# Kernel optimization log

Hardware: AMD Instinct MI355X
Metric: run time of the kernel (lower is better)

Reference implementation:

```python
import jax, jax.numpy as jnp
import numpy as np

EPS = 1e-6
RES_CONN = True


def _layernorm(x, g, b):
    mu = jnp.mean(x, axis=-1, keepdims=True)
    var = jnp.var(x, axis=-1, keepdims=True)
    return (x - mu) * jax.lax.rsqrt(var + EPS) * g + b


def setup_inputs() -> dict:
    key = jax.random.key(0)
    ks = jax.random.split(key, 8)
    L, H, V, B, T = 2, 1024, 32000, 4, 512
    s = 0.02
    return {
        "x": jax.random.randint(ks[0], (B, T), 0, V, dtype=jnp.int32),
        "emb": jax.random.normal(ks[1], (V, H), jnp.float32) * s,
        "ln_g": jnp.ones((L, H), jnp.float32),
        "ln_b": jnp.zeros((L, H), jnp.float32),
        "Wl": jax.random.normal(ks[2], (L, 2 * H, 4 * H), jnp.float32) * s,
        "bl": jnp.zeros((L, 4 * H), jnp.float32),
        "Wo": jax.random.normal(ks[3], (L, H, H), jnp.float32) * s,
        "bo": jnp.zeros((L, H), jnp.float32),
        "W1": jax.random.normal(ks[4], (L, H, 4 * H), jnp.float32) * s,
        "b1": jnp.zeros((L, 4 * H), jnp.float32),
        "W2": jax.random.normal(ks[5], (L, 4 * H, H), jnp.float32) * s,
        "b2": jnp.zeros((L, H), jnp.float32),
    }


def reference(x, emb, ln_g, ln_b, Wl, bl, Wo, bo, W1, b1, W2, b2):
    # x: [B, T] int token ids. Returns dec_logits [B, T, V].
    B, T = x.shape
    L, H = ln_g.shape
    x_emb = emb[x]                      # [B, T, H] (dropout inactive: eval mode)
    xs = jnp.swapaxes(x_emb, 0, 1)      # [T, B, H]

    def step(carry, xt):
        c_prev, h_prev = carry          # each [L, B, H]
        cs, hs = [], []
        prev_input = jnp.zeros_like(xt)
        inp = xt                        # [B, H]
        for m in range(L):
            xn = _layernorm(inp, ln_g[m], ln_b[m])
            z = jnp.concatenate([xn, h_prev[m]], axis=-1) @ Wl[m] + bl[m]
            z = z.reshape(B, 4, H)
            i_g = jax.nn.sigmoid(z[:, 0])
            f_g = jax.nn.sigmoid(z[:, 1])
            o_g = jax.nn.sigmoid(z[:, 2])
            c = f_g * c_prev[m] + i_g * jnp.tanh(z[:, 3])
            h = o_g * jnp.tanh(c)
            ff = jax.nn.relu(xn @ W1[m] + b1[m]) @ W2[m] + b2[m]
            y = inp + ff + h @ Wo[m] + bo[m]
            if RES_CONN:
                y = y + prev_input
            prev_input = inp
            inp = y
            cs.append(c)
            hs.append(h)
        logits = inp @ emb.T            # tied embedding: [B, V]
        return (jnp.stack(cs), jnp.stack(hs)), logits

    carry0 = (jnp.zeros((L, B, H), x_emb.dtype), jnp.zeros((L, B, H), x_emb.dtype))
    _, logits = jax.lax.scan(step, carry0, xs)   # logits [T, B, V]
    return jnp.swapaxes(logits, 0, 1)            # [B, T, V]
```

## Files before the change

### kernel.cpp

```cpp
#include <hip/hip_runtime.h>

typedef unsigned short u16;
typedef short bf16x8 __attribute__((ext_vector_type(8)));
typedef unsigned short ushort8 __attribute__((ext_vector_type(8)));
typedef unsigned short us4 __attribute__((ext_vector_type(4)));
typedef unsigned u32x4 __attribute__((ext_vector_type(4)));
typedef float fx4 __attribute__((ext_vector_type(4)));

#define DEVI __device__ __forceinline__

enum { BB = 4, TT = 512, HH = 1024, VV = 32000, H4 = 4096 };
enum { WSTR = 1032 };

DEVI u16 f2bf(float f) {
    union { float f; unsigned u; } x; x.f = f;
    unsigned r = x.u + 0x7fff + ((x.u >> 16) & 1);
    return (u16)(r >> 16);
}
DEVI float bf2f(u16 u) {
    union { unsigned u; float f; } x; x.u = ((unsigned)u) << 16;
    return x.f;
}
DEVI float sigm(float x) { return 1.f / (1.f + __expf(-x)); }

DEVI unsigned ald_u32(const unsigned* p) { return __hip_atomic_load(p, __ATOMIC_RELAXED, __HIP_MEMORY_SCOPE_AGENT); }
DEVI void ast_u32(unsigned* p, unsigned v) { __hip_atomic_store(p, v, __ATOMIC_RELAXED, __HIP_MEMORY_SCOPE_AGENT); }

DEVI void ld4cc(const unsigned* p, u32x4* out) {
    asm volatile("global_load_dwordx4 %0, %1, off sc0 sc1" : "=v"(*out) : "v"(p));
}

DEVI void poll4096(const unsigned* base, unsigned want, u16* st, int tid) {
    const unsigned* p0 = base + tid * 8;
    const unsigned* p1 = p0 + 4;
    u32x4 v0, v1;
    ld4cc(p0, &v0); ld4cc(p1, &v1);
    asm volatile("s_waitcnt vmcnt(0)" ::: "memory");
    __builtin_amdgcn_sched_barrier(0);
    for (;;) {
        bool o0 = ((v0[0]>>16)==want)&((v0[1]>>16)==want)&((v0[2]>>16)==want)&((v0[3]>>16)==want);
        bool o1 = ((v1[0]>>16)==want)&((v1[1]>>16)==want)&((v1[2]>>16)==want)&((v1[3]>>16)==want);
        if (o0 & o1) break;
        __builtin_amdgcn_s_sleep(4);
        if (!o0) ld4cc(p0, &v0);
        if (!o1) ld4cc(p1, &v1);
        asm volatile("s_waitcnt vmcnt(0)" ::: "memory");
        __builtin_amdgcn_sched_barrier(0);
    }
    int wi = tid * 8;
    u16* d = st + (wi >> 10) * WSTR + (wi & 1023);
    *(us4*)d       = (us4){(u16)v0[0], (u16)v0[1], (u16)v0[2], (u16)v0[3]};
    *(us4*)(d + 4) = (us4){(u16)v1[0], (u16)v1[1], (u16)v1[2], (u16)v1[3]};
}

DEVI unsigned poll_word(const unsigned* p, unsigned want) {
    unsigned v = ald_u32(p);
    while ((v >> 16) != want) { __builtin_amdgcn_s_sleep(2); v = ald_u32(p); }
    return v & 0xFFFFu;
}

DEVI void gates64(const u16* wl, const u16* st, float* fb, int tid) {
    int lane = tid & 63, wv = tid >> 6;
    int rt = wv & 3, kh = wv >> 2;
    fx4 acc = {0.f, 0.f, 0.f, 0.f};
    int aoff = (rt * 16 + (lane & 15)) * WSTR + (lane >> 4) * 8;
    int boff = (lane & 3) * WSTR + (lane >> 4) * 8;
#pragma unroll
    for (int kt = 0; kt < 16; kt++) {
        int k0 = (kh * 16 + kt) * 32;
        bf16x8 a = *(const bf16x8*)(wl + aoff + k0);
        bf16x8 b = *(const bf16x8*)(st + boff + k0);
        acc = __builtin_amdgcn_mfma_f32_16x16x32_bf16(a, b, acc, 0, 0, 0);
    }
    int col = lane & 15;
    if (col < 4) {
        int r0 = rt * 16 + (lane >> 4) * 4;
#pragma unroll
        for (int ri = 0; ri < 4; ri++) fb[kh * 256 + (r0 + ri) * 4 + col] = acc[ri];
    }
}

__global__ void transpose_cast(const float* __restrict__ src, u16* __restrict__ dst, int R, int C) {
    __shared__ float tile[32][33];
    int c0 = blockIdx.x * 32, r0 = blockIdx.y * 32;
    int x = threadIdx.x, y = threadIdx.y;
#pragma unroll
    for (int i = 0; i < 32; i += 8) tile[y + i][x] = src[(size_t)(r0 + y + i) * C + c0 + x];
    __syncthreads();
#pragma unroll
    for (int i = 0; i < 32; i += 8) dst[(size_t)(c0 + y + i) * R + r0 + x] = f2bf(tile[x][y + i]);
}

__global__ void cast_bf16(const float* __restrict__ src, u16* __restrict__ dst, int n) {
    int i = blockIdx.x * 256 + threadIdx.x;
    if (i < n) dst[i] = f2bf(src[i]);
}

__global__ void zero_buf(float* p, int n) {
    int i = blockIdx.x * 256 + threadIdx.x;
    if (i < n) p[i] = 0.f;
}

__global__ __launch_bounds__(256) void gather_ln(const int* __restrict__ x, const float* __restrict__ emb,
                                                 const float* __restrict__ g, const float* __restrict__ b,
                                                 float* __restrict__ xe, u16* __restrict__ xn0) {
    int t = blockIdx.x, bb = blockIdx.y;
    int row = x[bb * TT + t];
    const float* e = emb + (size_t)row * HH;
    float v[4]; float s = 0.f, s2 = 0.f;
#pragma unroll
    for (int p = 0; p < 4; p++) { v[p] = e[p * 256 + threadIdx.x]; s += v[p]; s2 += v[p] * v[p]; }
    __shared__ float ls[4], ls2[4];
    for (int off = 32; off; off >>= 1) { s += __shfl_xor(s, off); s2 += __shfl_xor(s2, off); }
    int w = threadIdx.x >> 6, lane = threadIdx.x & 63;
    if (lane == 0) { ls[w] = s; ls2[w] = s2; }
    __syncthreads();
    s = ls[0] + ls[1] + ls[2] + ls[3];
    s2 = ls2[0] + ls2[1] + ls2[2] + ls2[3];
    float mu = s * (1.f / HH);
    float var = s2 * (1.f / HH) - mu * mu;
    float rs = rsqrtf(var + 1e-6f);
    size_t base = ((size_t)t * BB + bb) * HH;
#pragma unroll
    for (int p = 0; p < 4; p++) {
        int j = p * 256 + threadIdx.x;
        xe[base + j] = v[p];
        xn0[base + j] = f2bf((v[p] - mu) * rs * g[j] + b[j]);
    }
}

template <int MODE>
__global__ __launch_bounds__(256) void gemm_bt(const u16* __restrict__ A, const u16* __restrict__ Bt,
                                               float* __restrict__ Cf, u16* __restrict__ Cb,
                                               const float* __restrict__ bias, int M, int N, int K) {
    __shared__ u16 ldsA[128 * 40];
    __shared__ u16 ldsB[128 * 40];
    const int tid = threadIdx.x;
    const int m0 = blockIdx.y * 128, n0 = blockIdx.x * 128;
    const int lane = tid & 63, wid = tid >> 6;
    const int wr = wid >> 1, wc = wid & 1;
    const int l15 = lane & 15, lk = (lane >> 4) * 8;
    fx4 acc[4][4];
#pragma unroll
    for (int a = 0; a < 4; a++)
#pragma unroll
        for (int b = 0; b < 4; b++) { fx4 z = {0.f, 0.f, 0.f, 0.f}; acc[a][b] = z; }

    const int arow = tid >> 2, acol = (tid & 3) * 8;
    for (int k0 = 0; k0 < K; k0 += 32) {
#pragma unroll
        for (int p = 0; p < 2; p++) {
            int r = arow + p * 64;
            ushort8 va = *(const ushort8*)(A + (size_t)(m0 + r) * K + k0 + acol);
            *(ushort8*)&ldsA[r * 40 + acol] = va;
            ushort8 vb = *(const ushort8*)(Bt + (size_t)(n0 + r) * K + k0 + acol);
            *(ushort8*)&ldsB[r * 40 + acol] = vb;
        }
        __syncthreads();
        bf16x8 af[4], bfr[4];
#pragma unroll
        for (int mi = 0; mi < 4; mi++) af[mi] = *(const bf16x8*)&ldsA[(wr * 64 + mi * 16 + l15) * 40 + lk];
#pragma unroll
        for (int ni = 0; ni < 4; ni++) bfr[ni] = *(const bf16x8*)&ldsB[(wc * 64 + ni * 16 + l15) * 40 + lk];
#pragma unroll
        for (int mi = 0; mi < 4; mi++)
#pragma unroll
            for (int ni = 0; ni < 4; ni++)
                acc[mi][ni] = __builtin_amdgcn_mfma_f32_16x16x32_bf16(af[mi], bfr[ni], acc[mi][ni], 0, 0, 0);
        __syncthreads();
    }
#pragma unroll
    for (int mi = 0; mi < 4; mi++) {
#pragma unroll
        for (int ni = 0; ni < 4; ni++) {
#pragma unroll
            for (int r = 0; r < 4; r++) {
                int gr = m0 + wr * 64 + mi * 16 + (lane >> 4) * 4 + r;
                int gc = n0 + wc * 64 + ni * 16 + l15;
                float v = acc[mi][ni][r];
                if (MODE == 0) {
                    Cf[(size_t)gr * N + gc] = v + bias[gc];
                } else if (MODE == 1) {
                    float u = v + bias[gc];
                    Cb[(size_t)gr * N + gc] = f2bf(u > 0.f ? u : 0.f);
                } else if (MODE == 2) {
                    Cf[(size_t)gr * N + gc] += v;
                } else {
                    int b = gr & 3, t = gr >> 2;
                    Cf[((size_t)b * TT + t) * VV + gc] = v;
                }
            }
        }
    }
}

__global__ __launch_bounds__(512, 1) void lstm_pipe(
    const u16* __restrict__ Wh0T, const u16* __restrict__ Wo0T,
    const u16* __restrict__ Wx1T, const u16* __restrict__ Wh1T,
    const float* __restrict__ pz_all, const float* __restrict__ xe, const float* __restrict__ ff0,
    const float* __restrict__ lng, const float* __restrict__ lnb,
    const float* __restrict__ bl, const float* __restrict__ bo,
    float* __restrict__ y0_all, u16* __restrict__ xn1, u16* __restrict__ H1bf,
    unsigned* __restrict__ R) {
    __shared__ u16 wlds[64 * WSTR];
    __shared__ u16 stg[4 * WSTR];
    __shared__ float fb[1664];

    const int bid = blockIdx.x;
    const int tid = threadIdx.x;

    unsigned* RH0 = R;
    unsigned* RH1 = R + 32768;
    unsigned* RPART = R + 49152;
    unsigned* RXN = R + 53248;
    unsigned* RZX = R + 118784;
    unsigned* PROGY = R + 380928;
    unsigned* PROGZX = R + 382976;
    unsigned* PROGL1 = R + 385024;

    if (bid < 64) {
        const int w = bid;
        {
            int row = tid >> 3, kc = tid & 7;
            int gr = (row >> 4) * 1024 + w * 16 + (row & 15);
            const uint4* s = (const uint4*)(Wh0T + (size_t)gr * 1024 + kc * 128);
            uint4* d = (uint4*)(wlds + row * WSTR + kc * 128);
#pragma unroll
            for (int i = 0; i < 16; i++) d[i] = s[i];
        }
        if (tid < 64) fb[1024 + tid] = 0.f;
        __syncthreads();

        for (int s = 0; s < TT; s++) {
            if ((s & 3) == 0 && tid < 64) {
                for (;;) {
                    unsigned p = ald_u32(PROGY + tid * 32);
#pragma unroll
                    for (int off = 1; off < 64; off <<= 1) {
                        unsigned o = (unsigned)__shfl_xor((int)p, off);
                        p = p < o ? p : o;
                    }
                    if ((int)p >= s - 4) break;
                    __builtin_amdgcn_s_sleep(8);
                }
            }
            float pzv[4] = {0.f, 0.f, 0.f, 0.f};
            if (tid < 64) {
                int x = tid >> 2, b = tid & 3;
#pragma unroll
                for (int g = 0; g < 4; g++)
                    pzv[g] = pz_all[((size_t)s * 4 + b) * 4096 + g * 1024 + w * 16 + x];
            }
            poll4096(RH0 + ((s + 7) & 7) * 4096, (unsigned)s, stg, tid);
            __syncthreads();
            float* gbuf = fb + (s & 1) * 512;
            gates64(wlds, stg, gbuf, tid);
            __syncthreads();
            if (tid < 64) {
                int x = tid >> 2, b = tid & 3;
                float z0 = gbuf[(0*16+x)*4+b] + gbuf[256+(0*16+x)*4+b] + pzv[0];
                float z1 = gbuf[(1*16+x)*4+b] + gbuf[256+(1*16+x)*4+b] + pzv[1];
                float z2 = gbuf[(2*16+x)*4+b] + gbuf[256+(2*16+x)*4+b] + pzv[2];
                float z3 = gbuf[(3*16+x)*4+b] + gbuf[256+(3*16+x)*4+b] + pzv[3];
                float ig = sigm(z0), fg = sigm(z1), og = sigm(z2), gg = tanhf(z3);
                float c = fg * fb[1024 + tid] + ig * gg;
                fb[1024 + tid] = c;
                float h = og * tanhf(c);
                ast_u32(&RH0[(s & 7) * 4096 + b * 1024 + w * 16 + x],
                        ((unsigned)(s + 1) << 16) | f2bf(h));
            }
        }
    } else if (bid < 128) {
        const int wy = bid - 64;
        {
            int row = tid >> 5, kc = tid & 31;
            const uint4* s = (const uint4*)(Wo0T + (size_t)(wy * 16 + row) * 1024 + kc * 32);
            uint4* d = (uint4*)(wlds + row * WSTR + kc * 32);
            d[0] = s[0]; d[1] = s[1]; d[2] = s[2]; d[3] = s[3];
        }
        float lgR = 0.f, lbR = 0.f, boR = 0.f;
        if (tid < 64) {
            int x = tid >> 2;
            lgR = lng[1024 + wy * 16 + x];
            lbR = lnb[1024 + wy * 16 + x];
            boR = bo[wy * 16 + x];
        }
        __syncthreads();

        for (int t = 0; t <= TT; t++) {
            const bool doDot = (t < TT);
            const bool doLN = (t >= 1);
            if ((t & 7) == 0 && tid < 64) {
                for (;;) {
                    unsigned p = ald_u32(PROGZX + tid * 32);
#pragma unroll
                    for (int off = 1; off < 64; off <<= 1) {
                        unsigned o = (unsigned)__shfl_xor((int)p, off);
                        p = p < o ? p : o;
                    }
                    if ((int)p >= t - 8) break;
                    __builtin_amdgcn_s_sleep(8);
                }
            }
            float xev = 0.f, ffv = 0.f;
            if (doDot && tid < 64) {
                int x = tid >> 2, b = tid & 3;
                size_t base = ((size_t)t * 4 + b) * 1024 + wy * 16 + x;
                xev = xe[base]; ffv = ff0[base];
            }
            if (doDot) poll4096(RH0 + (t & 7) * 4096, (unsigned)(t + 1), stg, tid);
            __syncthreads();
            if (doDot && tid == 0) ast_u32(PROGY + wy * 32, (unsigned)(t + 1));
            if (doDot) {
                int out = tid >> 3, c = tid & 7;
                const u16* wrow = wlds + (out >> 2) * WSTR + c * 128;
                const u16* hrow = stg + (out & 3) * WSTR + c * 128;
                float acc = 0.f;
#pragma unroll
                for (int m = 0; m < 16; m++) {
                    ushort8 w8 = *(const ushort8*)(wrow + m * 8);
                    ushort8 h8 = *(const ushort8*)(hrow + m * 8);
#pragma unroll
                    for (int q = 0; q < 8; q++) acc += bf2f(w8[q]) * bf2f(h8[q]);
                }
                acc += __shfl_xor(acc, 1); acc += __shfl_xor(acc, 2); acc += __shfl_xor(acc, 4);
                if (c == 0) fb[512 + out] = acc;
            }
            if (doLN) {
                const unsigned* p = RPART + ((t - 1) & 3) * 1024 + tid * 2;
                unsigned hi = poll_word(p, (unsigned)t);
                unsigned lo = poll_word(p + 1, (unsigned)t);
                union { unsigned u; float f; } cv; cv.u = (hi << 16) | lo;
                fb[tid] = cv.f;
            }
            __syncthreads();
            if (doLN && tid < 8) {
                int b = tid & 3, kind = tid >> 2;
                float S = 0.f;
                for (int i = 0; i < 64; i++) S += fb[i * 8 + b * 2 + kind];
                fb[704 + kind * 4 + b] = S;
            }
            if (doDot && tid < 64) {
                int x = tid >> 2, b = tid & 3;
                float y = fb[512 + tid] + xev + ffv + boR;
                y0_all[((size_t)t * 4 + b) * 1024 + wy * 16 + x] = y;
                fb[576 + (t & 1) * 64 + tid] = y;
                float sv = y, sq = y * y;
#pragma unroll
                for (int off = 4; off < 64; off <<= 1) { sv += __shfl_xor(sv, off); sq += __shfl_xor(sq, off); }
                if (tid < 4) {
                    unsigned tg = (unsigned)(t + 1) << 16;
                    unsigned* pb = RPART + (t & 3) * 1024 + wy * 16 + tid * 4;
                    union { float f; unsigned u; } c1, c2; c1.f = sv; c2.f = sq;
                    ast_u32(pb + 0, tg | (c1.u >> 16));
                    ast_u32(pb + 1, tg | (c1.u & 0xFFFFu));
                    ast_u32(pb + 2, tg | (c2.u >> 16));
                    ast_u32(pb + 3, tg | (c2.u & 0xFFFFu));
                }
            }
            __syncthreads();
            if (doLN && tid < 64) {
                int x = tid >> 2, b = tid & 3;
                int u = t - 1;
                float mu = fb[704 + b] * (1.f / 1024.f);
                float rs = rsqrtf(fb[708 + b] * (1.f / 1024.f) - mu * mu + 1e-6f);
                float yv = fb[576 + (u & 1) * 64 + tid];
                float xnv = (yv - mu) * rs * lgR + lbR;
                u16 xb = f2bf(xnv);
                xn1[(size_t)u * 4096 + b * 1024 + wy * 16 + x] = xb;
                ast_u32(&RXN[(u & 15) * 4096 + b * 1024 + wy * 16 + x],
                        ((unsigned)(u + 1) << 16) | xb);
            }
        }
    } else if (bid < 192) {
        const int wz = bid - 128;
        {
            int row = tid >> 3, kc = tid & 7;
            int gr = (row >> 4) * 1024 + wz * 16 + (row & 15);
            const uint4* s = (const uint4*)(Wx1T + (size_t)gr * 1024 + kc * 128);
            uint4* d = (uint4*)(wlds + row * WSTR + kc * 128);
#pragma unroll
            for (int i = 0; i < 16; i++) d[i] = s[i];
        }
        if (tid < 64) fb[1536 + tid] = bl[4096 + (tid >> 4) * 1024 + wz * 16 + (tid & 15)];
        __syncthreads();

        for (int t = 0; t < TT; t++) {
            if ((t & 7) == 0 && tid == 0) {
                while ((int)ald_u32(PROGL1) < t - 6) __builtin_amdgcn_s_sleep(8);
            }
            poll4096(RXN + (t & 15) * 4096, (unsigned)(t + 1), stg, tid);
            __syncthreads();
            gates64(wlds, stg, fb, tid);
            __syncthreads();
            if (tid == 0) ast_u32(PROGZX + wz * 32, (unsigned)(t + 1));
            if (tid < 256) {
                int lr = tid >> 2, b = tid & 3;
                float v = fb[lr * 4 + b] + fb[256 + lr * 4 + b] + fb[1536 + lr];
                ast_u32(&RZX[(t & 15) * 16384 + wz * 256 + tid],
                        ((unsigned)(t + 1) << 16) | f2bf(v));
            }
            __syncthreads();
        }
    } else {
        const int w1 = bid - 192;
        {
            int row = tid >> 3, kc = tid & 7;
            int gr = (row >> 4) * 1024 + w1 * 16 + (row & 15);
            const uint4* s = (const uint4*)(Wh1T + (size_t)gr * 1024 + kc * 128);
            uint4* d = (uint4*)(wlds + row * WSTR + kc * 128);
#pragma unroll
            for (int i = 0; i < 16; i++) d[i] = s[i];
        }
        if (tid < 64) fb[1600 + tid] = 0.f;
        __syncthreads();

        for (int v = 0; v < TT; v++) {
            poll4096(RH1 + ((v + 3) & 3) * 4096, (unsigned)v, stg, tid);
            if (tid < 256) {
                const unsigned* p = RZX + (v & 15) * 16384 + w1 * 256 + tid;
                fb[1024 + (v & 1) * 256 + tid] = bf2f((u16)poll_word(p, (unsigned)(v + 1)));
            }
            __syncthreads();
            if (bid == 192 && tid == 0) ast_u32(PROGL1, (unsigned)(v + 1));
            float* gbuf = fb + (v & 1) * 512;
            gates64(wlds, stg, gbuf, tid);
            __syncthreads();
            if (tid < 64) {
                int x = tid >> 2, b = tid & 3;
                const float* zb = fb + 1024 + (v & 1) * 256;
                float z0 = gbuf[(0*16+x)*4+b] + gbuf[256+(0*16+x)*4+b] + zb[(0*16+x)*4+b];
                float z1 = gbuf[(1*16+x)*4+b] + gbuf[256+(1*16+x)*4+b] + zb[(1*16+x)*4+b];
                float z2 = gbuf[(2*16+x)*4+b] + gbuf[256+(2*16+x)*4+b] + zb[(2*16+x)*4+b];
                float z3 = gbuf[(3*16+x)*4+b] + gbuf[256+(3*16+x)*4+b] + zb[(3*16+x)*4+b];
                float ig = sigm(z0), fg = sigm(z1), og = sigm(z2), gg = tanhf(z3);
                float c = fg * fb[1600 + tid] + ig * gg;
                fb[1600 + tid] = c;
                float h = og * tanhf(c);
                u16 hb = f2bf(h);
                H1bf[(size_t)v * 4096 + b * 1024 + w1 * 16 + x] = hb;
                ast_u32(&RH1[(v & 3) * 4096 + b * 1024 + w1 * 16 + x],
                        ((unsigned)(v + 1) << 16) | hb);
            }
        }
    }
}

__global__ void p1_add(float* __restrict__ y, const float* __restrict__ xe,
                       const float* __restrict__ b2_1, const float* __restrict__ bo_1) {
    int idx = blockIdx.x * 256 + threadIdx.x;
    int j = idx & (HH - 1);
    y[idx] += xe[idx] + b2_1[j] + bo_1[j];
}

__global__ void p2_cast(const float* __restrict__ y, u16* __restrict__ o) {
    int idx = blockIdx.x * 256 + threadIdx.x;
    o[idx] = f2bf(y[idx]);
}

extern "C" void kernel_launch(void* const* d_in, const int* in_sizes, int n_in,
                              void* d_out, int out_size, void* d_ws, size_t ws_size,
                              hipStream_t stream) {
    const int* x = (const int*)d_in[0];
    const float* emb = (const float*)d_in[1];
    const float* ln_g = (const float*)d_in[2];
    const float* ln_b = (const float*)d_in[3];
    const float* Wl = (const float*)d_in[4];
    const float* bl = (const float*)d_in[5];
    const float* Wo = (const float*)d_in[6];
    const float* bo = (const float*)d_in[7];
    const float* W1 = (const float*)d_in[8];
    const float* b1 = (const float*)d_in[9];
    const float* W2 = (const float*)d_in[10];
    const float* b2 = (const float*)d_in[11];
    float* out = (float*)d_out;

    char* wp = (char*)d_ws;
    auto alloc = [&](size_t bytes) { void* p = wp; wp += (bytes + 255) & ~(size_t)255; return p; };
    const size_t MBT = (size_t)TT * BB;
    float* xe     = (float*)alloc(MBT * HH * 4);
    float* pre_z0 = (float*)alloc(MBT * H4 * 4);
    float* ff0    = (float*)alloc(MBT * HH * 4);
    float* y0_all = (float*)alloc(MBT * HH * 4);
    u16* xn0      = (u16*)alloc(MBT * HH * 2);
    u16* xn1      = (u16*)alloc(MBT * HH * 2);
    u16* U0       = (u16*)alloc(MBT * H4 * 2);
    u16* U1       = (u16*)alloc(MBT * H4 * 2);
    u16* H1bf     = (u16*)alloc(MBT * HH * 2);
    u16* Y1bf     = (u16*)alloc(MBT * HH * 2);
    unsigned* R   = (unsigned*)alloc(385056 * 4);
    u16* WlxT0 = (u16*)alloc((size_t)H4 * HH * 2);
    u16* WlhT0 = (u16*)alloc((size_t)H4 * HH * 2);
    u16* WlxT1 = (u16*)alloc((size_t)H4 * HH * 2);
    u16* WlhT1 = (u16*)alloc((size_t)H4 * HH * 2);
    u16* Wo0T  = (u16*)alloc((size_t)HH * HH * 2);
    u16* Wo1T  = (u16*)alloc((size_t)HH * HH * 2);
    u16* W10T  = (u16*)alloc((size_t)H4 * HH * 2);
    u16* W11T  = (u16*)alloc((size_t)H4 * HH * 2);
    u16* W20T  = (u16*)alloc((size_t)HH * H4 * 2);
    u16* W21T  = (u16*)alloc((size_t)HH * H4 * 2);
    u16* embB  = (u16*)alloc((size_t)VV * HH * 2);

    dim3 tb(32, 8);
    transpose_cast<<<dim3(128, 32), tb, 0, stream>>>(Wl, WlxT0, HH, H4);
    transpose_cast<<<dim3(128, 32), tb, 0, stream>>>(Wl + 1024 * 4096, WlhT0, HH, H4);
    transpose_cast<<<dim3(128, 32), tb, 0, stream>>>(Wl + 2048 * 4096, WlxT1, HH, H4);
    transpose_cast<<<dim3(128, 32), tb, 0, stream>>>(Wl + 3072 * 4096, WlhT1, HH, H4);
    transpose_cast<<<dim3(32, 32), tb, 0, stream>>>(Wo, Wo0T, HH, HH);
    transpose_cast<<<dim3(32, 32), tb, 0, stream>>>(Wo + 1024 * 1024, Wo1T, HH, HH);
    transpose_cast<<<dim3(128, 32), tb, 0, stream>>>(W1, W10T, HH, H4);
    transpose_cast<<<dim3(128, 32), tb, 0, stream>>>(W1 + 1024 * 4096, W11T, HH, H4);
    transpose_cast<<<dim3(32, 128), tb, 0, stream>>>(W2, W20T, H4, HH);
    transpose_cast<<<dim3(32, 128), tb, 0, stream>>>(W2 + 4096 * 1024, W21T, H4, HH);
    cast_bf16<<<(VV * HH + 255) / 256, 256, 0, stream>>>(emb, embB, VV * HH);
    gather_ln<<<dim3(TT, BB), 256, 0, stream>>>(x, emb, ln_g, ln_b, xe, xn0);

    gemm_bt<0><<<dim3(32, 16), 256, 0, stream>>>(xn0, WlxT0, pre_z0, nullptr, bl, 2048, 4096, 1024);
    gemm_bt<1><<<dim3(32, 16), 256, 0, stream>>>(xn0, W10T, nullptr, U0, b1, 2048, 4096, 1024);
    gemm_bt<0><<<dim3(8, 16), 256, 0, stream>>>(U0, W20T, ff0, nullptr, b2, 2048, 1024, 4096);

    zero_buf<<<1505, 256, 0, stream>>>((float*)R, 385056);

    lstm_pipe<<<256, 512, 0, stream>>>(WlhT0, Wo0T, WlxT1, WlhT1, pre_z0, xe, ff0,
                                       ln_g, ln_b, bl, bo, y0_all, xn1, H1bf, R);

    gemm_bt<1><<<dim3(32, 16), 256, 0, stream>>>(xn1, W11T, nullptr, U1, b1 + 4096, 2048, 4096, 1024);
    p1_add<<<8192, 256, 0, stream>>>(y0_all, xe, b2 + 1024, bo + 1024);
    gemm_bt<2><<<dim3(8, 16), 256, 0, stream>>>(U1, W21T, y0_all, nullptr, nullptr, 2048, 1024, 4096);
    gemm_bt<2><<<dim3(8, 16), 256, 0, stream>>>(H1bf, Wo1T, y0_all, nullptr, nullptr, 2048, 1024, 1024);
    p2_cast<<<8192, 256, 0, stream>>>(y0_all, Y1bf);
    gemm_bt<3><<<dim3(250, 16), 256, 0, stream>>>(Y1bf, embB, out, nullptr, nullptr, 2048, 32000, 1024);
}
```

Baseline: 3.693 ms.

## Replace per-element tagged h exchange with packed data plus per-block sentinel flags

Hidden-state exchange between LSTM blocks moves from per-element tagged 32-bit words (a step tag in the high half) to packed bf16 pairs plus a per-block sentinel array. Consumers poll 64 sentinels with one wave, then fetch the data once, instead of spin-polling all 4096 tagged words. This cuts polling traffic and halves the data size, at the cost of a store fence (waitcnt) before each sentinel write. It also deepens the ring buffer to 16 slots with a looser throttle, adds a custom tanh, tunes sleep intervals, and moves the Wo dot product after the layer-norm partial-sum wait so the two overlap.

```diff
diff --git a/kernel.cpp b/kernel.cpp
--- a/kernel.cpp
+++ b/kernel.cpp
@@ -22,6 +22,11 @@
     return x.f;
 }
 DEVI float sigm(float x) { return 1.f / (1.f + __expf(-x)); }
+DEVI float tanh_f(float x) {
+    float a = fabsf(x);
+    float t = 1.f - 2.f / (__expf(2.f * a) + 1.f);
+    return x < 0.f ? -t : t;
+}
 
 DEVI unsigned ald_u32(const unsigned* p) { return __hip_atomic_load(p, __ATOMIC_RELAXED, __HIP_MEMORY_SCOPE_AGENT); }
 DEVI void ast_u32(unsigned* p, unsigned v) { __hip_atomic_store(p, v, __ATOMIC_RELAXED, __HIP_MEMORY_SCOPE_AGENT); }
@@ -30,6 +35,24 @@
     asm volatile("global_load_dwordx4 %0, %1, off sc0 sc1" : "=v"(*out) : "v"(p));
 }
 
+template <int SLP>
+DEVI void sent_poll(const unsigned* sbase, unsigned want, int lane) {
+    const unsigned* p = sbase + lane;
+    unsigned v = ald_u32(p);
+    while (v != want) { __builtin_amdgcn_s_sleep(SLP); v = ald_u32(p); }
+}
+DEVI void data_fetch(const unsigned* dbase, u16* st, int tid) {
+    u32x4 d;
+    ld4cc(dbase + tid * 4, &d);
+    asm volatile("s_waitcnt vmcnt(0)" ::: "memory");
+    __builtin_amdgcn_sched_barrier(0);
+    int wi = tid * 8;
+    u16* dst = st + (wi >> 10) * WSTR + (wi & 1023);
+    *(us4*)dst       = (us4){(u16)d[0], (u16)(d[0] >> 16), (u16)d[1], (u16)(d[1] >> 16)};
+    *(us4*)(dst + 4) = (us4){(u16)d[2], (u16)(d[2] >> 16), (u16)d[3], (u16)(d[3] >> 16)};
+}
+
+template <int SLP>
 DEVI void poll4096(const unsigned* base, unsigned want, u16* st, int tid) {
     const unsigned* p0 = base + tid * 8;
     const unsigned* p1 = p0 + 4;
@@ -41,7 +64,7 @@
         bool o0 = ((v0[0]>>16)==want)&((v0[1]>>16)==want)&((v0[2]>>16)==want)&((v0[3]>>16)==want);
         bool o1 = ((v1[0]>>16)==want)&((v1[1]>>16)==want)&((v1[2]>>16)==want)&((v1[3]>>16)==want);
         if (o0 & o1) break;
-        __builtin_amdgcn_s_sleep(4);
+        __builtin_amdgcn_s_sleep(SLP);
         if (!o0) ld4cc(p0, &v0);
         if (!o1) ld4cc(p1, &v1);
         asm volatile("s_waitcnt vmcnt(0)" ::: "memory");
@@ -208,15 +231,18 @@
 
     const int bid = blockIdx.x;
     const int tid = threadIdx.x;
-
-    unsigned* RH0 = R;
-    unsigned* RH1 = R + 32768;
-    unsigned* RPART = R + 49152;
-    unsigned* RXN = R + 53248;
-    unsigned* RZX = R + 118784;
-    unsigned* PROGY = R + 380928;
-    unsigned* PROGZX = R + 382976;
-    unsigned* PROGL1 = R + 385024;
+    const int lane = tid & 63, wv = tid >> 6;
+
+    unsigned* RD0 = R;
+    unsigned* RS0 = R + 32768;
+    unsigned* RD1 = R + 33792;
+    unsigned* RS1 = R + 41984;
+    unsigned* RPART = R + 42240;
+    unsigned* RXN = R + 46336;
+    unsigned* RZX = R + 111872;
+    unsigned* PROGY = R + 374016;
+    unsigned* PROGZX = R + 376064;
+    unsigned* PROGL1 = R + 378112;
 
     if (bid < 64) {
         const int w = bid;
@@ -232,7 +258,7 @@
         __syncthreads();
 
         for (int s = 0; s < TT; s++) {
-            if ((s & 3) == 0 && tid < 64) {
+            if ((s & 7) == 0 && tid < 64) {
                 for (;;) {
                     unsigned p = ald_u32(PROGY + tid * 32);
 #pragma unroll
@@ -240,7 +266,7 @@
                         unsigned o = (unsigned)__shfl_xor((int)p, off);
                         p = p < o ? p : o;
                     }
-                    if ((int)p >= s - 4) break;
+                    if ((int)p >= s - 8) break;
                     __builtin_amdgcn_s_sleep(8);
                 }
             }
@@ -251,7 +277,9 @@
                 for (int g = 0; g < 4; g++)
                     pzv[g] = pz_all[((size_t)s * 4 + b) * 4096 + g * 1024 + w * 16 + x];
             }
-            poll4096(RH0 + ((s + 7) & 7) * 4096, (unsigned)s, stg, tid);
+            if (wv == 0) sent_poll<1>(RS0 + ((s + 15) & 15) * 64, (unsigned)s, lane);
+            __syncthreads();
+            data_fetch(RD0 + ((s + 15) & 15) * 2048, stg, tid);
             __syncthreads();
             float* gbuf = fb + (s & 1) * 512;
             gates64(wlds, stg, gbuf, tid);
@@ -262,12 +290,18 @@
                 float z1 = gbuf[(1*16+x)*4+b] + gbuf[256+(1*16+x)*4+b] + pzv[1];
                 float z2 = gbuf[(2*16+x)*4+b] + gbuf[256+(2*16+x)*4+b] + pzv[2];
                 float z3 = gbuf[(3*16+x)*4+b] + gbuf[256+(3*16+x)*4+b] + pzv[3];
-                float ig = sigm(z0), fg = sigm(z1), og = sigm(z2), gg = tanhf(z3);
+                float ig = sigm(z0), fg = sigm(z1), og = sigm(z2), gg = tanh_f(z3);
                 float c = fg * fb[1024 + tid] + ig * gg;
                 fb[1024 + tid] = c;
-                float h = og * tanhf(c);
-                ast_u32(&RH0[(s & 7) * 4096 + b * 1024 + w * 16 + x],
-                        ((unsigned)(s + 1) << 16) | f2bf(h));
+                float h = og * tanh_f(c);
+                float hn = __shfl(h, (tid + 4) & 63);
+                if (((tid >> 2) & 1) == 0) {
+                    int x = tid >> 2, b = tid & 3;
+                    unsigned word = (unsigned)f2bf(h) | ((unsigned)f2bf(hn) << 16);
+                    ast_u32(&RD0[(s & 15) * 2048 + b * 512 + w * 8 + (x >> 1)], word);
+                }
+                asm volatile("s_waitcnt vmcnt(0)" ::: "memory");
+                if (tid == 0) ast_u32(&RS0[(s & 15) * 64 + w], (unsigned)(s + 1));
             }
         }
     } else if (bid < 128) {
@@ -308,24 +342,9 @@
                 size_t base = ((size_t)t * 4 + b) * 1024 + wy * 16 + x;
                 xev = xe[base]; ffv = ff0[base];
             }
-            if (doDot) poll4096(RH0 + (t & 7) * 4096, (unsigned)(t + 1), stg, tid);
-            __syncthreads();
-            if (doDot && tid == 0) ast_u32(PROGY + wy * 32, (unsigned)(t + 1));
-            if (doDot) {
-                int out = tid >> 3, c = tid & 7;
-                const u16* wrow = wlds + (out >> 2) * WSTR + c * 128;
-                const u16* hrow = stg + (out & 3) * WSTR + c * 128;
-                float acc = 0.f;
-#pragma unroll
-                for (int m = 0; m < 16; m++) {
-                    ushort8 w8 = *(const ushort8*)(wrow + m * 8);
-                    ushort8 h8 = *(const ushort8*)(hrow + m * 8);
-#pragma unroll
-                    for (int q = 0; q < 8; q++) acc += bf2f(w8[q]) * bf2f(h8[q]);
-                }
-                acc += __shfl_xor(acc, 1); acc += __shfl_xor(acc, 2); acc += __shfl_xor(acc, 4);
-                if (c == 0) fb[512 + out] = acc;
-            }
+            if (doDot && wv == 0) sent_poll<4>(RS0 + (t & 15) * 64, (unsigned)(t + 1), lane);
+            __syncthreads();
+            if (doDot) data_fetch(RD0 + (t & 15) * 2048, stg, tid);
             if (doLN) {
                 const unsigned* p = RPART + ((t - 1) & 3) * 1024 + tid * 2;
                 unsigned hi = poll_word(p, (unsigned)t);
@@ -334,12 +353,29 @@
                 fb[tid] = cv.f;
             }
             __syncthreads();
+            if (doDot && tid == 0) ast_u32(PROGY + wy * 32, (unsigned)(t + 1));
             if (doLN && tid < 8) {
                 int b = tid & 3, kind = tid >> 2;
                 float S = 0.f;
                 for (int i = 0; i < 64; i++) S += fb[i * 8 + b * 2 + kind];
                 fb[704 + kind * 4 + b] = S;
             }
+            if (doDot) {
+                int out = tid >> 3, c = tid & 7;
+                const u16* wrow = wlds + (out >> 2) * WSTR + c * 128;
+                const u16* hrow = stg + (out & 3) * WSTR + c * 128;
+                float acc = 0.f;
+#pragma unroll
+                for (int m = 0; m < 16; m++) {
+                    ushort8 w8 = *(const ushort8*)(wrow + m * 8);
+                    ushort8 h8 = *(const ushort8*)(hrow + m * 8);
+#pragma unroll
+                    for (int q = 0; q < 8; q++) acc += bf2f(w8[q]) * bf2f(h8[q]);
+                }
+                acc += __shfl_xor(acc, 1); acc += __shfl_xor(acc, 2); acc += __shfl_xor(acc, 4);
+                if (c == 0) fb[512 + out] = acc;
+            }
+            __syncthreads();
             if (doDot && tid < 64) {
                 int x = tid >> 2, b = tid & 3;
                 float y = fb[512 + tid] + xev + ffv + boR;
@@ -389,7 +425,7 @@
             if ((t & 7) == 0 && tid == 0) {
                 while ((int)ald_u32(PROGL1) < t - 6) __builtin_amdgcn_s_sleep(8);
             }
-            poll4096(RXN + (t & 15) * 4096, (unsigned)(t + 1), stg, tid);
+            poll4096<8>(RXN + (t & 15) * 4096, (unsigned)(t + 1), stg, tid);
             __syncthreads();
             gates64(wlds, stg, fb, tid);
             __syncthreads();
@@ -416,11 +452,13 @@
         __syncthreads();
 
         for (int v = 0; v < TT; v++) {
-            poll4096(RH1 + ((v + 3) & 3) * 4096, (unsigned)v, stg, tid);
             if (tid < 256) {
                 const unsigned* p = RZX + (v & 15) * 16384 + w1 * 256 + tid;
                 fb[1024 + (v & 1) * 256 + tid] = bf2f((u16)poll_word(p, (unsigned)(v + 1)));
             }
+            if (wv == 0) sent_poll<1>(RS1 + ((v + 3) & 3) * 64, (unsigned)v, lane);
+            __syncthreads();
+            data_fetch(RD1 + ((v + 3) & 3) * 2048, stg, tid);
             __syncthreads();
             if (bid == 192 && tid == 0) ast_u32(PROGL1, (unsigned)(v + 1));
             float* gbuf = fb + (v & 1) * 512;
@@ -433,14 +471,19 @@
                 float z1 = gbuf[(1*16+x)*4+b] + gbuf[256+(1*16+x)*4+b] + zb[(1*16+x)*4+b];
                 float z2 = gbuf[(2*16+x)*4+b] + gbuf[256+(2*16+x)*4+b] + zb[(2*16+x)*4+b];
                 float z3 = gbuf[(3*16+x)*4+b] + gbuf[256+(3*16+x)*4+b] + zb[(3*16+x)*4+b];
-                float ig = sigm(z0), fg = sigm(z1), og = sigm(z2), gg = tanhf(z3);
+                float ig = sigm(z0), fg = sigm(z1), og = sigm(z2), gg = tanh_f(z3);
                 float c = fg * fb[1600 + tid] + ig * gg;
                 fb[1600 + tid] = c;
-                float h = og * tanhf(c);
+                float h = og * tanh_f(c);
                 u16 hb = f2bf(h);
                 H1bf[(size_t)v * 4096 + b * 1024 + w1 * 16 + x] = hb;
-                ast_u32(&RH1[(v & 3) * 4096 + b * 1024 + w1 * 16 + x],
-                        ((unsigned)(v + 1) << 16) | hb);
+                float hn = __shfl(h, (tid + 4) & 63);
+                if (((tid >> 2) & 1) == 0) {
+                    unsigned word = (unsigned)hb | ((unsigned)f2bf(hn) << 16);
+                    ast_u32(&RD1[(v & 3) * 2048 + b * 512 + w1 * 8 + ((tid >> 2) >> 1)], word);
+                }
+                asm volatile("s_waitcnt vmcnt(0)" ::: "memory");
+                if (tid == 0) ast_u32(&RS1[(v & 3) * 64 + w1], (unsigned)(v + 1));
             }
         }
     }
@@ -488,7 +531,7 @@
     u16* U1       = (u16*)alloc(MBT * H4 * 2);
     u16* H1bf     = (u16*)alloc(MBT * HH * 2);
     u16* Y1bf     = (u16*)alloc(MBT * HH * 2);
-    unsigned* R   = (unsigned*)alloc(385056 * 4);
+    unsigned* R   = (unsigned*)alloc(378144 * 4);
     u16* WlxT0 = (u16*)alloc((size_t)H4 * HH * 2);
     u16* WlhT0 = (u16*)alloc((size_t)H4 * HH * 2);
     u16* WlxT1 = (u16*)alloc((size_t)H4 * HH * 2);
@@ -519,7 +562,7 @@
     gemm_bt<1><<<dim3(32, 16), 256, 0, stream>>>(xn0, W10T, nullptr, U0, b1, 2048, 4096, 1024);
     gemm_bt<0><<<dim3(8, 16), 256, 0, stream>>>(U0, W20T, ff0, nullptr, b2, 2048, 1024, 4096);
 
-    zero_buf<<<1505, 256, 0, stream>>>((float*)R, 385056);
+    zero_buf<<<1478, 256, 0, stream>>>((float*)R, 378144);
 
     lstm_pipe<<<256, 512, 0, stream>>>(WlhT0, Wo0T, WlxT1, WlhT1, pre_z0, xe, ff0,
                                        ln_g, ln_b, bl, bo, y0_all, xn1, H1bf, R);
```

New measurement: 3.641 ms. About the same (-1.4%).
